# Performance work log

Measured on AMD Instinct MI355X. Metric: run time of the kernel, lower is better.

The kernel has to match this reference:

```python
import jax, jax.numpy as jnp
import numpy as np

B, S, D, H = 4, 2048, 512, 8
HD = D // H  # head dim = 64


def setup_inputs() -> dict:
    key = jax.random.key(0)
    ks = jax.random.split(key, 7)
    s = 0.02
    return {
        "X": jax.random.normal(ks[0], (B, S, D), dtype=jnp.float32),
        "Y": jax.random.normal(ks[1], (B, S, D), dtype=jnp.float32),
        "Z": jax.random.normal(ks[2], (B, S, D), dtype=jnp.float32),
        # weights stored as [in, out] (torch Linear weight transposed)
        "Wq": jax.random.normal(ks[3], (D, D), dtype=jnp.float32) * s,
        "Wk": jax.random.normal(ks[4], (D, D), dtype=jnp.float32) * s,
        "Wv": jax.random.normal(ks[5], (D, D), dtype=jnp.float32) * s,  # dead in original forward
        "Wo": jax.random.normal(ks[6], (D, D), dtype=jnp.float32) * s,
    }


def _split_heads(t):
    # [B, S, D] -> [B, H, S, HD]
    return t.reshape(B, S, H, HD).transpose(0, 2, 1, 3)


def reference(X, Y, Z, Wq, Wk, Wv, Wo):
    q = _split_heads(X @ Wq)
    k = _split_heads(Y @ Wk)
    # NOTE: original module (faithfully) uses W_o for the value projection; W_v is unused.
    v = _split_heads(Z @ Wo)
    scores = jnp.einsum("bhqd,bhkd->bhqk", q, k) / jnp.sqrt(jnp.float32(HD))
    # sigmoid(s) > 0.5  <=>  s > 0 (sigmoid strictly monotone); keep score else 0
    scores = jnp.where(scores > 0, scores, jnp.float32(0))
    attn = jax.nn.softmax(scores, axis=-1)
    out = jnp.einsum("bhqk,bhkd->bhqd", attn, v)  # dropout inactive at eval
    out = out.transpose(0, 2, 1, 3).reshape(B, S, D)  # merge heads
    return out @ Wo
```

## Files before the change

### kernel.cpp

```cpp
#include <hip/hip_runtime.h>
#include <math.h>

#define S_LEN 2048
#define DIM   512
#define M_TOT 8192
#define NCH   (S_LEN / 64)

typedef __attribute__((ext_vector_type(8))) short bf16x8;
typedef __attribute__((ext_vector_type(4))) short bf16x4;
typedef __attribute__((ext_vector_type(4))) float f32x4;

#define MFMA(a, b, c) __builtin_amdgcn_mfma_f32_16x16x32_bf16((a), (b), (c), 0, 0, 0)

#define QSCALE 0.18033688011112042f

__device__ __forceinline__ short f2b(float x) {
    union { float f; unsigned u; } v; v.f = x;
    unsigned r = v.u + 0x7FFFu + ((v.u >> 16) & 1u);
    return (short)(r >> 16);
}

__device__ __forceinline__ unsigned cvtpk(float a, float b) {
    unsigned r;
    asm("v_cvt_pk_bf16_f32 %0, %1, %2" : "=v"(r) : "v"(a), "v"(b));
    return r;
}

__device__ __forceinline__ bf16x8 cvt8(float4 lo, float4 hi) {
    union { unsigned u[4]; bf16x8 v; } o;
    o.u[0] = cvtpk(lo.x, lo.y);
    o.u[1] = cvtpk(lo.z, lo.w);
    o.u[2] = cvtpk(hi.x, hi.y);
    o.u[3] = cvtpk(hi.z, hi.w);
    return o.v;
}

__device__ __forceinline__ float fast_exp2(float x) {
#if __has_builtin(__builtin_amdgcn_exp2f)
    return __builtin_amdgcn_exp2f(x);
#else
    return __expf(x * 0.693147180559945f);
#endif
}

__global__ __launch_bounds__(256) void prep_wt(const float* Wq, const float* Wk, const float* Wo,
                                               short* Wtq, short* Wtk, short* Wto) {
    const int zi = blockIdx.z;
    const float* W = zi == 0 ? Wq : zi == 1 ? Wk : Wo;
    short*      Wt = zi == 0 ? Wtq : zi == 1 ? Wtk : Wto;
    const float sc = zi == 0 ? QSCALE : 1.0f;
    __shared__ short Ts[64 * 72];
    const int t = threadIdx.x;
    const int k0 = blockIdx.x * 64, n0 = blockIdx.y * 64;
    #pragma unroll
    for (int it = 0; it < 4; ++it) {
        const int r = (t >> 4) + 16 * it;
        const int cq = t & 15;
        float4 v = *(const float4*)&W[(size_t)(k0 + r) * DIM + n0 + cq * 4];
        Ts[(4 * cq + 0) * 72 + r] = f2b(v.x * sc);
        Ts[(4 * cq + 1) * 72 + r] = f2b(v.y * sc);
        Ts[(4 * cq + 2) * 72 + r] = f2b(v.z * sc);
        Ts[(4 * cq + 3) * 72 + r] = f2b(v.w * sc);
    }
    __syncthreads();
    #pragma unroll
    for (int it = 0; it < 2; ++it) {
        const int n = (t >> 3) + 32 * it;
        const int sg = t & 7;
        *(bf16x8*)&Wt[(size_t)(n0 + n) * DIM + k0 + sg * 8] = *(const bf16x8*)&Ts[n * 72 + sg * 8];
    }
}

__global__ __launch_bounds__(256) void proj_gemm(const float* __restrict__ X,
                                                 const float* __restrict__ Y,
                                                 const float* __restrict__ Z,
                                                 const short* __restrict__ Wtq,
                                                 const short* __restrict__ Wtk,
                                                 const short* __restrict__ Wto,
                                                 short* __restrict__ Qb,
                                                 short* __restrict__ Kb,
                                                 short* __restrict__ Vt) {
    const int zi = blockIdx.z;
    const float* A  = zi == 0 ? X : zi == 1 ? Y : Z;
    const short* Bw = zi == 0 ? Wtq : zi == 1 ? Wtk : Wto;

    __shared__ short As[128 * 40];
    __shared__ short Bs[128 * 40];
    const int tid = threadIdx.x;
    const int w = tid >> 6, ln = tid & 63, l15 = ln & 15, quad = ln >> 4;
    const int m0 = blockIdx.x * 128, n0 = blockIdx.y * 128;
    const int wm = (w & 1) * 64, wn = (w >> 1) * 64;

    const int r0 = tid >> 2, r1 = r0 + 64;
    const int sg = tid & 3;
    const float* ap0 = A  + (size_t)(m0 + r0) * DIM + sg * 8;
    const float* ap1 = A  + (size_t)(m0 + r1) * DIM + sg * 8;
    const short* bp0 = Bw + (size_t)(n0 + r0) * DIM + sg * 8;
    const short* bp1 = Bw + (size_t)(n0 + r1) * DIM + sg * 8;

    float4 a0l = *(const float4*)ap0, a0h = *(const float4*)(ap0 + 4);
    float4 a1l = *(const float4*)ap1, a1h = *(const float4*)(ap1 + 4);
    bf16x8 b0 = *(const bf16x8*)bp0, b1 = *(const bf16x8*)bp1;

    f32x4 acc[4][4] = {};

    for (int k0 = 0; k0 < DIM; k0 += 32) {
        __syncthreads();
        *(bf16x8*)&As[r0 * 40 + sg * 8] = cvt8(a0l, a0h);
        *(bf16x8*)&As[r1 * 40 + sg * 8] = cvt8(a1l, a1h);
        *(bf16x8*)&Bs[r0 * 40 + sg * 8] = b0;
        *(bf16x8*)&Bs[r1 * 40 + sg * 8] = b1;
        __syncthreads();
        const int kn = (k0 + 32 < DIM) ? k0 + 32 : 0;
        a0l = *(const float4*)(ap0 + kn); a0h = *(const float4*)(ap0 + kn + 4);
        a1l = *(const float4*)(ap1 + kn); a1h = *(const float4*)(ap1 + kn + 4);
        b0 = *(const bf16x8*)(bp0 + kn); b1 = *(const bf16x8*)(bp1 + kn);

        bf16x8 af[4], bf[4];
        #pragma unroll
        for (int mf = 0; mf < 4; ++mf) af[mf] = *(const bf16x8*)&As[(wm + 16 * mf + l15) * 40 + quad * 8];
        #pragma unroll
        for (int nf = 0; nf < 4; ++nf) bf[nf] = *(const bf16x8*)&Bs[(wn + 16 * nf + l15) * 40 + quad * 8];
        #pragma unroll
        for (int mf = 0; mf < 4; ++mf)
            #pragma unroll
            for (int nf = 0; nf < 4; ++nf)
                acc[mf][nf] = MFMA(af[mf], bf[nf], acc[mf][nf]);
    }

    if (zi < 2) {
        short* C = zi == 0 ? Qb : Kb;
        #pragma unroll
        for (int mf = 0; mf < 4; ++mf)
            #pragma unroll
            for (int nf = 0; nf < 4; ++nf)
                #pragma unroll
                for (int r = 0; r < 4; ++r)
                    C[(size_t)(m0 + wm + 16 * mf + 4 * quad + r) * DIM + n0 + wn + 16 * nf + l15] =
                        f2b(acc[mf][nf][r]);
    } else {
        #pragma unroll
        for (int mf = 0; mf < 4; ++mf)
            #pragma unroll
            for (int nf = 0; nf < 4; ++nf) {
                const int col = n0 + wn + 16 * nf + l15;
                const int h = col >> 6, hd = col & 63;
                const int row0_ = m0 + wm + 16 * mf + 4 * quad;
                const int bb = row0_ >> 11, s0 = row0_ & 2047;
                bf16x4 o = { f2b(acc[mf][nf][0]), f2b(acc[mf][nf][1]),
                             f2b(acc[mf][nf][2]), f2b(acc[mf][nf][3]) };
                *(bf16x4*)&Vt[((size_t)((bb * 8 + h) * 64 + hd)) * S_LEN + s0] = o;
            }
    }
}

__global__ __launch_bounds__(256) void out_gemm(const short* __restrict__ Ob,
                                                const short* __restrict__ Wto,
                                                float* __restrict__ Cout) {
    __shared__ short As[128 * 40];
    __shared__ short Bs[128 * 40];
    const int tid = threadIdx.x;
    const int w = tid >> 6, ln = tid & 63, l15 = ln & 15, quad = ln >> 4;
    const int m0 = blockIdx.x * 128, n0 = blockIdx.y * 128;
    const int wm = (w & 1) * 64, wn = (w >> 1) * 64;

    const int r0 = tid >> 2, r1 = r0 + 64;
    const int sg = tid & 3;
    const short* ap0 = Ob  + (size_t)(m0 + r0) * DIM + sg * 8;
    const short* ap1 = Ob  + (size_t)(m0 + r1) * DIM + sg * 8;
    const short* bp0 = Wto + (size_t)(n0 + r0) * DIM + sg * 8;
    const short* bp1 = Wto + (size_t)(n0 + r1) * DIM + sg * 8;

    bf16x8 a0 = *(const bf16x8*)ap0, a1 = *(const bf16x8*)ap1;
    bf16x8 b0 = *(const bf16x8*)bp0, b1 = *(const bf16x8*)bp1;

    f32x4 acc[4][4] = {};

    for (int k0 = 0; k0 < DIM; k0 += 32) {
        __syncthreads();
        *(bf16x8*)&As[r0 * 40 + sg * 8] = a0;
        *(bf16x8*)&As[r1 * 40 + sg * 8] = a1;
        *(bf16x8*)&Bs[r0 * 40 + sg * 8] = b0;
        *(bf16x8*)&Bs[r1 * 40 + sg * 8] = b1;
        __syncthreads();
        const int kn = (k0 + 32 < DIM) ? k0 + 32 : 0;
        a0 = *(const bf16x8*)(ap0 + kn); a1 = *(const bf16x8*)(ap1 + kn);
        b0 = *(const bf16x8*)(bp0 + kn); b1 = *(const bf16x8*)(bp1 + kn);

        bf16x8 af[4], bf[4];
        #pragma unroll
        for (int mf = 0; mf < 4; ++mf) af[mf] = *(const bf16x8*)&As[(wm + 16 * mf + l15) * 40 + quad * 8];
        #pragma unroll
        for (int nf = 0; nf < 4; ++nf) bf[nf] = *(const bf16x8*)&Bs[(wn + 16 * nf + l15) * 40 + quad * 8];
        #pragma unroll
        for (int mf = 0; mf < 4; ++mf)
            #pragma unroll
            for (int nf = 0; nf < 4; ++nf)
                acc[mf][nf] = MFMA(af[mf], bf[nf], acc[mf][nf]);
    }
    #pragma unroll
    for (int mf = 0; mf < 4; ++mf)
        #pragma unroll
        for (int nf = 0; nf < 4; ++nf)
            #pragma unroll
            for (int r = 0; r < 4; ++r)
                Cout[(size_t)(m0 + wm + 16 * mf + 4 * quad + r) * DIM + n0 + wn + 16 * nf + l15] =
                    acc[mf][nf][r];
}

__global__ __launch_bounds__(256) void attn_mfma(const short* __restrict__ Qb,
                                                 const short* __restrict__ Kb,
                                                 const short* __restrict__ Vtg,
                                                 short* __restrict__ Ob) {
    __shared__ short Ks[2][64 * 72];
    __shared__ short Vs[2][64 * 72];
    __shared__ short Es[4][32 * 72];

    const int tid = threadIdx.x;
    const int w = tid >> 6, ln = tid & 63, l15 = ln & 15, quad = ln >> 4;

    const int lin = blockIdx.y * 16 + blockIdx.x;
    const int swz = ((lin & 7) << 6) + (lin >> 3);
    const int qt0 = (swz & 15) * 128;
    const int bh  = swz >> 4;
    const int b = bh >> 3, h = bh & 7;
    const size_t tokbase = (size_t)b * S_LEN;

    bf16x8 qf[2][2];
    #pragma unroll
    for (int nf = 0; nf < 2; ++nf)
        #pragma unroll
        for (int ks = 0; ks < 2; ++ks)
            qf[nf][ks] = *(const bf16x8*)&Qb[(tokbase + qt0 + 32 * w + 16 * nf + l15) * DIM +
                                             h * 64 + 32 * ks + 8 * quad];

    const int srow = tid >> 3, ssg = tid & 7;
    const short* kbase = Kb  + (tokbase + srow) * DIM + h * 64 + ssg * 8;
    const short* vbase = Vtg + ((size_t)bh * 64 + srow) * S_LEN + ssg * 8;

    bf16x8 k0r, k1r, v0r, v1r;

    f32x4 oacc[2][4] = {};
    f32x4 d4[2] = {};

    {
        k0r = *(const bf16x8*)kbase;
        k1r = *(const bf16x8*)(kbase + (size_t)32 * DIM);
        v0r = *(const bf16x8*)vbase;
        v1r = *(const bf16x8*)(vbase + (size_t)32 * S_LEN);
        *(bf16x8*)&Ks[0][srow * 72 + ssg * 8] = k0r;
        *(bf16x8*)&Ks[0][(srow + 32) * 72 + ssg * 8] = k1r;
        *(bf16x8*)&Vs[0][srow * 72 + ssg * 8] = v0r;
        *(bf16x8*)&Vs[0][(srow + 32) * 72 + ssg * 8] = v1r;
        k0r = *(const bf16x8*)(kbase + (size_t)64 * DIM);
        k1r = *(const bf16x8*)(kbase + (size_t)96 * DIM);
        v0r = *(const bf16x8*)(vbase + 64);
        v1r = *(const bf16x8*)(vbase + (size_t)32 * S_LEN + 64);
    }
    __syncthreads();

    for (int kc = 0; kc < NCH; ++kc) {
        const int cur = kc & 1;
        if (kc + 1 < NCH) {
            *(bf16x8*)&Ks[cur ^ 1][srow * 72 + ssg * 8] = k0r;
            *(bf16x8*)&Ks[cur ^ 1][(srow + 32) * 72 + ssg * 8] = k1r;
            *(bf16x8*)&Vs[cur ^ 1][srow * 72 + ssg * 8] = v0r;
            *(bf16x8*)&Vs[cur ^ 1][(srow + 32) * 72 + ssg * 8] = v1r;
        }
        if (kc + 2 < NCH) {
            const size_t ko = (size_t)(kc + 2) * 64 * DIM;
            const size_t vo = (size_t)(kc + 2) * 64;
            k0r = *(const bf16x8*)(kbase + ko);
            k1r = *(const bf16x8*)(kbase + ko + (size_t)32 * DIM);
            v0r = *(const bf16x8*)(vbase + vo);
            v1r = *(const bf16x8*)(vbase + vo + (size_t)32 * S_LEN);
        }

        f32x4 sacc[4][2];
        __builtin_amdgcn_s_setprio(1);
        #pragma unroll
        for (int mf = 0; mf < 4; ++mf) {
            bf16x8 ka = *(const bf16x8*)&Ks[cur][(16 * mf + l15) * 72 + 8 * quad];
            bf16x8 kb = *(const bf16x8*)&Ks[cur][(16 * mf + l15) * 72 + 32 + 8 * quad];
            #pragma unroll
            for (int nf = 0; nf < 2; ++nf) {
                f32x4 s = {0.f, 0.f, 0.f, 0.f};
                s = MFMA(ka, qf[nf][0], s);
                s = MFMA(kb, qf[nf][1], s);
                sacc[mf][nf] = s;
            }
        }
        __builtin_amdgcn_s_setprio(0);

        short* Esw = &Es[w][0];
        #pragma unroll
        for (int mf = 0; mf < 4; ++mf)
            #pragma unroll
            for (int nf = 0; nf < 2; ++nf) {
                const float e0 = fast_exp2(fmaxf(sacc[mf][nf][0], 0.f));
                const float e1 = fast_exp2(fmaxf(sacc[mf][nf][1], 0.f));
                const float e2 = fast_exp2(fmaxf(sacc[mf][nf][2], 0.f));
                const float e3 = fast_exp2(fmaxf(sacc[mf][nf][3], 0.f));
                d4[nf][0] += e0; d4[nf][1] += e1;
                d4[nf][2] += e2; d4[nf][3] += e3;
                uint2 p;
                p.x = cvtpk(e0, e1);
                p.y = cvtpk(e2, e3);
                *(uint2*)&Esw[(16 * nf + l15) * 72 + 16 * mf + 4 * quad] = p;
            }

        bf16x8 e00 = *(const bf16x8*)&Esw[l15 * 72 + 8 * quad];
        bf16x8 e01 = *(const bf16x8*)&Esw[l15 * 72 + 32 + 8 * quad];
        bf16x8 e10 = *(const bf16x8*)&Esw[(16 + l15) * 72 + 8 * quad];
        bf16x8 e11 = *(const bf16x8*)&Esw[(16 + l15) * 72 + 32 + 8 * quad];
        __builtin_amdgcn_s_setprio(1);
        #pragma unroll
        for (int nf2 = 0; nf2 < 4; ++nf2) {
            bf16x8 vf0 = *(const bf16x8*)&Vs[cur][(16 * nf2 + l15) * 72 + 8 * quad];
            bf16x8 vf1 = *(const bf16x8*)&Vs[cur][(16 * nf2 + l15) * 72 + 32 + 8 * quad];
            oacc[0][nf2] = MFMA(e00, vf0, oacc[0][nf2]);
            oacc[0][nf2] = MFMA(e01, vf1, oacc[0][nf2]);
            oacc[1][nf2] = MFMA(e10, vf0, oacc[1][nf2]);
            oacc[1][nf2] = MFMA(e11, vf1, oacc[1][nf2]);
        }
        __builtin_amdgcn_s_setprio(0);
        __syncthreads();
    }

    float dsum[2];
    #pragma unroll
    for (int nf = 0; nf < 2; ++nf) {
        dsum[nf] = (d4[nf][0] + d4[nf][1]) + (d4[nf][2] + d4[nf][3]);
        dsum[nf] += __shfl_xor(dsum[nf], 16);
        dsum[nf] += __shfl_xor(dsum[nf], 32);
    }
    const float dinv0 = 1.0f / dsum[0];
    const float dinv1 = 1.0f / dsum[1];

    #pragma unroll
    for (int mf2 = 0; mf2 < 2; ++mf2) {
        const float dv = mf2 ? dinv1 : dinv0;
        #pragma unroll
        for (int r = 0; r < 4; ++r) {
            const float di = __shfl(dv, 4 * quad + r);
            const size_t rowaddr = (tokbase + qt0 + 32 * w + 16 * mf2 + 4 * quad + r) * DIM + h * 64;
            #pragma unroll
            for (int nf2 = 0; nf2 < 4; ++nf2)
                Ob[rowaddr + 16 * nf2 + l15] = f2b(oacc[mf2][nf2][r] * di);
        }
    }
}

extern "C" void kernel_launch(void* const* d_in, const int* in_sizes, int n_in,
                              void* d_out, int out_size, void* d_ws, size_t ws_size,
                              hipStream_t stream) {
    const float* X  = (const float*)d_in[0];
    const float* Y  = (const float*)d_in[1];
    const float* Z  = (const float*)d_in[2];
    const float* Wq = (const float*)d_in[3];
    const float* Wk = (const float*)d_in[4];
    const float* Wo = (const float*)d_in[6];

    char* p = (char*)d_ws;
    const size_t MD = (size_t)M_TOT * DIM;
    short* Qb  = (short*)p; p += MD * 2;
    short* Kb  = (short*)p; p += MD * 2;
    short* Vt  = (short*)p; p += MD * 2;
    short* Ob  = (short*)p; p += MD * 2;
    short* Wtq = (short*)p; p += (size_t)DIM * DIM * 2;
    short* Wtk = (short*)p; p += (size_t)DIM * DIM * 2;
    short* Wto = (short*)p; p += (size_t)DIM * DIM * 2;

    prep_wt<<<dim3(8, 8, 3), 256, 0, stream>>>(Wq, Wk, Wo, Wtq, Wtk, Wto);
    proj_gemm<<<dim3(64, 4, 3), 256, 0, stream>>>(X, Y, Z, Wtq, Wtk, Wto, Qb, Kb, Vt);
    attn_mfma<<<dim3(16, 32), 256, 0, stream>>>(Qb, Kb, Vt, Ob);
    out_gemm<<<dim3(64, 4), 256, 0, stream>>>(Ob, Wto, (float*)d_out);
}
```

Before: 208.7 us.

## Halve attention and output GEMM tiles to double grid size, drop LDS double-buffering

The attention kernel now gives each block 64 queries instead of 128 (16 per wave), launching 1024 blocks with a 1D swizzled index, and replaces the double-buffered K/V shared tiles with a single buffer plus a register prefetch one chunk ahead. The output GEMM tile shrinks from 128x128 to 64x64 with 1024 swizzled blocks. This is meant to raise occupancy and fill the CUs better with less LDS and fewer registers per block. In exchange, each K/V tile is loaded from global twice as often per query, MFMA work per LDS read drops, and removing the double buffer exposes load latency at each barrier.

```diff
diff --git a/kernel.cpp b/kernel.cpp
--- a/kernel.cpp
+++ b/kernel.cpp
@@ -157,51 +157,48 @@
 __global__ __launch_bounds__(256) void out_gemm(const short* __restrict__ Ob,
                                                 const short* __restrict__ Wto,
                                                 float* __restrict__ Cout) {
-    __shared__ short As[128 * 40];
-    __shared__ short Bs[128 * 40];
+    __shared__ short As[64 * 40];
+    __shared__ short Bs[64 * 40];
     const int tid = threadIdx.x;
     const int w = tid >> 6, ln = tid & 63, l15 = ln & 15, quad = ln >> 4;
-    const int m0 = blockIdx.x * 128, n0 = blockIdx.y * 128;
-    const int wm = (w & 1) * 64, wn = (w >> 1) * 64;
-
-    const int r0 = tid >> 2, r1 = r0 + 64;
+
+    const int f = blockIdx.x;
+    const int swz = ((f & 7) << 7) | (f >> 3);
+    const int m0 = (swz >> 3) * 64, n0 = (swz & 7) * 64;
+    const int wm = (w & 1) * 32, wn = (w >> 1) * 32;
+
+    const int row = tid >> 2;
     const int sg = tid & 3;
-    const short* ap0 = Ob  + (size_t)(m0 + r0) * DIM + sg * 8;
-    const short* ap1 = Ob  + (size_t)(m0 + r1) * DIM + sg * 8;
-    const short* bp0 = Wto + (size_t)(n0 + r0) * DIM + sg * 8;
-    const short* bp1 = Wto + (size_t)(n0 + r1) * DIM + sg * 8;
-
-    bf16x8 a0 = *(const bf16x8*)ap0, a1 = *(const bf16x8*)ap1;
-    bf16x8 b0 = *(const bf16x8*)bp0, b1 = *(const bf16x8*)bp1;
-
-    f32x4 acc[4][4] = {};
+    const short* ap = Ob  + (size_t)(m0 + row) * DIM + sg * 8;
+    const short* bp = Wto + (size_t)(n0 + row) * DIM + sg * 8;
+
+    bf16x8 a0 = *(const bf16x8*)ap, b0 = *(const bf16x8*)bp;
+
+    f32x4 acc[2][2] = {};
 
     for (int k0 = 0; k0 < DIM; k0 += 32) {
         __syncthreads();
-        *(bf16x8*)&As[r0 * 40 + sg * 8] = a0;
-        *(bf16x8*)&As[r1 * 40 + sg * 8] = a1;
-        *(bf16x8*)&Bs[r0 * 40 + sg * 8] = b0;
-        *(bf16x8*)&Bs[r1 * 40 + sg * 8] = b1;
+        *(bf16x8*)&As[row * 40 + sg * 8] = a0;
+        *(bf16x8*)&Bs[row * 40 + sg * 8] = b0;
         __syncthreads();
         const int kn = (k0 + 32 < DIM) ? k0 + 32 : 0;
-        a0 = *(const bf16x8*)(ap0 + kn); a1 = *(const bf16x8*)(ap1 + kn);
-        b0 = *(const bf16x8*)(bp0 + kn); b1 = *(const bf16x8*)(bp1 + kn);
-
-        bf16x8 af[4], bf[4];
-        #pragma unroll
-        for (int mf = 0; mf < 4; ++mf) af[mf] = *(const bf16x8*)&As[(wm + 16 * mf + l15) * 40 + quad * 8];
-        #pragma unroll
-        for (int nf = 0; nf < 4; ++nf) bf[nf] = *(const bf16x8*)&Bs[(wn + 16 * nf + l15) * 40 + quad * 8];
-        #pragma unroll
-        for (int mf = 0; mf < 4; ++mf)
-            #pragma unroll
-            for (int nf = 0; nf < 4; ++nf)
+        a0 = *(const bf16x8*)(ap + kn); b0 = *(const bf16x8*)(bp + kn);
+
+        bf16x8 af[2], bf[2];
+        #pragma unroll
+        for (int mf = 0; mf < 2; ++mf) af[mf] = *(const bf16x8*)&As[(wm + 16 * mf + l15) * 40 + quad * 8];
+        #pragma unroll
+        for (int nf = 0; nf < 2; ++nf) bf[nf] = *(const bf16x8*)&Bs[(wn + 16 * nf + l15) * 40 + quad * 8];
+        #pragma unroll
+        for (int mf = 0; mf < 2; ++mf)
+            #pragma unroll
+            for (int nf = 0; nf < 2; ++nf)
                 acc[mf][nf] = MFMA(af[mf], bf[nf], acc[mf][nf]);
     }
     #pragma unroll
-    for (int mf = 0; mf < 4; ++mf)
-        #pragma unroll
-        for (int nf = 0; nf < 4; ++nf)
+    for (int mf = 0; mf < 2; ++mf)
+        #pragma unroll
+        for (int nf = 0; nf < 2; ++nf)
             #pragma unroll
             for (int r = 0; r < 4; ++r)
                 Cout[(size_t)(m0 + wm + 16 * mf + 4 * quad + r) * DIM + n0 + wn + 16 * nf + l15] =
@@ -212,142 +209,106 @@
                                                  const short* __restrict__ Kb,
                                                  const short* __restrict__ Vtg,
                                                  short* __restrict__ Ob) {
-    __shared__ short Ks[2][64 * 72];
-    __shared__ short Vs[2][64 * 72];
-    __shared__ short Es[4][32 * 72];
+    __shared__ short Ks[64 * 72];
+    __shared__ short Vs[64 * 72];
+    __shared__ short Es[4][16 * 72];
 
     const int tid = threadIdx.x;
     const int w = tid >> 6, ln = tid & 63, l15 = ln & 15, quad = ln >> 4;
 
-    const int lin = blockIdx.y * 16 + blockIdx.x;
-    const int swz = ((lin & 7) << 6) + (lin >> 3);
-    const int qt0 = (swz & 15) * 128;
-    const int bh  = swz >> 4;
+    const int f = blockIdx.x;
+    const int swz = ((f & 7) << 7) | (f >> 3);
+    const int qt0 = (swz & 31) * 64;
+    const int bh  = swz >> 5;
     const int b = bh >> 3, h = bh & 7;
     const size_t tokbase = (size_t)b * S_LEN;
 
-    bf16x8 qf[2][2];
-    #pragma unroll
-    for (int nf = 0; nf < 2; ++nf)
-        #pragma unroll
-        for (int ks = 0; ks < 2; ++ks)
-            qf[nf][ks] = *(const bf16x8*)&Qb[(tokbase + qt0 + 32 * w + 16 * nf + l15) * DIM +
-                                             h * 64 + 32 * ks + 8 * quad];
+    bf16x8 qf[2];
+    #pragma unroll
+    for (int ks = 0; ks < 2; ++ks)
+        qf[ks] = *(const bf16x8*)&Qb[(tokbase + qt0 + 16 * w + l15) * DIM +
+                                     h * 64 + 32 * ks + 8 * quad];
 
     const int srow = tid >> 3, ssg = tid & 7;
     const short* kbase = Kb  + (tokbase + srow) * DIM + h * 64 + ssg * 8;
     const short* vbase = Vtg + ((size_t)bh * 64 + srow) * S_LEN + ssg * 8;
 
-    bf16x8 k0r, k1r, v0r, v1r;
-
-    f32x4 oacc[2][4] = {};
-    f32x4 d4[2] = {};
-
-    {
-        k0r = *(const bf16x8*)kbase;
-        k1r = *(const bf16x8*)(kbase + (size_t)32 * DIM);
-        v0r = *(const bf16x8*)vbase;
-        v1r = *(const bf16x8*)(vbase + (size_t)32 * S_LEN);
-        *(bf16x8*)&Ks[0][srow * 72 + ssg * 8] = k0r;
-        *(bf16x8*)&Ks[0][(srow + 32) * 72 + ssg * 8] = k1r;
-        *(bf16x8*)&Vs[0][srow * 72 + ssg * 8] = v0r;
-        *(bf16x8*)&Vs[0][(srow + 32) * 72 + ssg * 8] = v1r;
-        k0r = *(const bf16x8*)(kbase + (size_t)64 * DIM);
-        k1r = *(const bf16x8*)(kbase + (size_t)96 * DIM);
-        v0r = *(const bf16x8*)(vbase + 64);
-        v1r = *(const bf16x8*)(vbase + (size_t)32 * S_LEN + 64);
-    }
-    __syncthreads();
+    bf16x8 k0r = *(const bf16x8*)kbase;
+    bf16x8 k1r = *(const bf16x8*)(kbase + (size_t)32 * DIM);
+    bf16x8 v0r = *(const bf16x8*)vbase;
+    bf16x8 v1r = *(const bf16x8*)(vbase + (size_t)32 * S_LEN);
+
+    f32x4 oacc[4] = {};
+    f32x4 d4 = {0.f, 0.f, 0.f, 0.f};
 
     for (int kc = 0; kc < NCH; ++kc) {
-        const int cur = kc & 1;
+        *(bf16x8*)&Ks[srow * 72 + ssg * 8] = k0r;
+        *(bf16x8*)&Ks[(srow + 32) * 72 + ssg * 8] = k1r;
+        *(bf16x8*)&Vs[srow * 72 + ssg * 8] = v0r;
+        *(bf16x8*)&Vs[(srow + 32) * 72 + ssg * 8] = v1r;
+        __syncthreads();
         if (kc + 1 < NCH) {
-            *(bf16x8*)&Ks[cur ^ 1][srow * 72 + ssg * 8] = k0r;
-            *(bf16x8*)&Ks[cur ^ 1][(srow + 32) * 72 + ssg * 8] = k1r;
-            *(bf16x8*)&Vs[cur ^ 1][srow * 72 + ssg * 8] = v0r;
-            *(bf16x8*)&Vs[cur ^ 1][(srow + 32) * 72 + ssg * 8] = v1r;
-        }
-        if (kc + 2 < NCH) {
-            const size_t ko = (size_t)(kc + 2) * 64 * DIM;
-            const size_t vo = (size_t)(kc + 2) * 64;
+            const size_t ko = (size_t)(kc + 1) * 64 * DIM;
+            const size_t vo = (size_t)(kc + 1) * 64;
             k0r = *(const bf16x8*)(kbase + ko);
             k1r = *(const bf16x8*)(kbase + ko + (size_t)32 * DIM);
             v0r = *(const bf16x8*)(vbase + vo);
             v1r = *(const bf16x8*)(vbase + vo + (size_t)32 * S_LEN);
         }
 
-        f32x4 sacc[4][2];
+        f32x4 sacc[4];
         __builtin_amdgcn_s_setprio(1);
         #pragma unroll
         for (int mf = 0; mf < 4; ++mf) {
-            bf16x8 ka = *(const bf16x8*)&Ks[cur][(16 * mf + l15) * 72 + 8 * quad];
-            bf16x8 kb = *(const bf16x8*)&Ks[cur][(16 * mf + l15) * 72 + 32 + 8 * quad];
-            #pragma unroll
-            for (int nf = 0; nf < 2; ++nf) {
-                f32x4 s = {0.f, 0.f, 0.f, 0.f};
-                s = MFMA(ka, qf[nf][0], s);
-                s = MFMA(kb, qf[nf][1], s);
-                sacc[mf][nf] = s;
-            }
+            bf16x8 ka = *(const bf16x8*)&Ks[(16 * mf + l15) * 72 + 8 * quad];
+            bf16x8 kb = *(const bf16x8*)&Ks[(16 * mf + l15) * 72 + 32 + 8 * quad];
+            f32x4 s = {0.f, 0.f, 0.f, 0.f};
+            s = MFMA(ka, qf[0], s);
+            s = MFMA(kb, qf[1], s);
+            sacc[mf] = s;
         }
         __builtin_amdgcn_s_setprio(0);
 
         short* Esw = &Es[w][0];
         #pragma unroll
-        for (int mf = 0; mf < 4; ++mf)
-            #pragma unroll
-            for (int nf = 0; nf < 2; ++nf) {
-                const float e0 = fast_exp2(fmaxf(sacc[mf][nf][0], 0.f));
-                const float e1 = fast_exp2(fmaxf(sacc[mf][nf][1], 0.f));
-                const float e2 = fast_exp2(fmaxf(sacc[mf][nf][2], 0.f));
-                const float e3 = fast_exp2(fmaxf(sacc[mf][nf][3], 0.f));
-                d4[nf][0] += e0; d4[nf][1] += e1;
-                d4[nf][2] += e2; d4[nf][3] += e3;
-                uint2 p;
-                p.x = cvtpk(e0, e1);
-                p.y = cvtpk(e2, e3);
-                *(uint2*)&Esw[(16 * nf + l15) * 72 + 16 * mf + 4 * quad] = p;
-            }
-
-        bf16x8 e00 = *(const bf16x8*)&Esw[l15 * 72 + 8 * quad];
-        bf16x8 e01 = *(const bf16x8*)&Esw[l15 * 72 + 32 + 8 * quad];
-        bf16x8 e10 = *(const bf16x8*)&Esw[(16 + l15) * 72 + 8 * quad];
-        bf16x8 e11 = *(const bf16x8*)&Esw[(16 + l15) * 72 + 32 + 8 * quad];
+        for (int mf = 0; mf < 4; ++mf) {
+            const float e0 = fast_exp2(fmaxf(sacc[mf][0], 0.f));
+            const float e1 = fast_exp2(fmaxf(sacc[mf][1], 0.f));
+            const float e2 = fast_exp2(fmaxf(sacc[mf][2], 0.f));
+            const float e3 = fast_exp2(fmaxf(sacc[mf][3], 0.f));
+            d4[0] += e0; d4[1] += e1; d4[2] += e2; d4[3] += e3;
+            uint2 p;
+            p.x = cvtpk(e0, e1);
+            p.y = cvtpk(e2, e3);
+            *(uint2*)&Esw[l15 * 72 + 16 * mf + 4 * quad] = p;
+        }
+
+        bf16x8 e0 = *(const bf16x8*)&Esw[l15 * 72 + 8 * quad];
+        bf16x8 e1 = *(const bf16x8*)&Esw[l15 * 72 + 32 + 8 * quad];
         __builtin_amdgcn_s_setprio(1);
         #pragma unroll
         for (int nf2 = 0; nf2 < 4; ++nf2) {
-            bf16x8 vf0 = *(const bf16x8*)&Vs[cur][(16 * nf2 + l15) * 72 + 8 * quad];
-            bf16x8 vf1 = *(const bf16x8*)&Vs[cur][(16 * nf2 + l15) * 72 + 32 + 8 * quad];
-            oacc[0][nf2] = MFMA(e00, vf0, oacc[0][nf2]);
-            oacc[0][nf2] = MFMA(e01, vf1, oacc[0][nf2]);
-            oacc[1][nf2] = MFMA(e10, vf0, oacc[1][nf2]);
-            oacc[1][nf2] = MFMA(e11, vf1, oacc[1][nf2]);
+            bf16x8 vf0 = *(const bf16x8*)&Vs[(16 * nf2 + l15) * 72 + 8 * quad];
+            bf16x8 vf1 = *(const bf16x8*)&Vs[(16 * nf2 + l15) * 72 + 32 + 8 * quad];
+            oacc[nf2] = MFMA(e0, vf0, oacc[nf2]);
+            oacc[nf2] = MFMA(e1, vf1, oacc[nf2]);
         }
         __builtin_amdgcn_s_setprio(0);
         __syncthreads();
     }
 
-    float dsum[2];
-    #pragma unroll
-    for (int nf = 0; nf < 2; ++nf) {
-        dsum[nf] = (d4[nf][0] + d4[nf][1]) + (d4[nf][2] + d4[nf][3]);
-        dsum[nf] += __shfl_xor(dsum[nf], 16);
-        dsum[nf] += __shfl_xor(dsum[nf], 32);
-    }
-    const float dinv0 = 1.0f / dsum[0];
-    const float dinv1 = 1.0f / dsum[1];
-
-    #pragma unroll
-    for (int mf2 = 0; mf2 < 2; ++mf2) {
-        const float dv = mf2 ? dinv1 : dinv0;
-        #pragma unroll
-        for (int r = 0; r < 4; ++r) {
-            const float di = __shfl(dv, 4 * quad + r);
-            const size_t rowaddr = (tokbase + qt0 + 32 * w + 16 * mf2 + 4 * quad + r) * DIM + h * 64;
-            #pragma unroll
-            for (int nf2 = 0; nf2 < 4; ++nf2)
-                Ob[rowaddr + 16 * nf2 + l15] = f2b(oacc[mf2][nf2][r] * di);
-        }
+    float dsum = (d4[0] + d4[1]) + (d4[2] + d4[3]);
+    dsum += __shfl_xor(dsum, 16);
+    dsum += __shfl_xor(dsum, 32);
+    const float dinv = 1.0f / dsum;
+
+    #pragma unroll
+    for (int r = 0; r < 4; ++r) {
+        const float di = __shfl(dinv, 4 * quad + r);
+        const size_t rowaddr = (tokbase + qt0 + 16 * w + 4 * quad + r) * DIM + h * 64;
+        #pragma unroll
+        for (int nf2 = 0; nf2 < 4; ++nf2)
+            Ob[rowaddr + 16 * nf2 + l15] = f2b(oacc[nf2][r] * di);
     }
 }
 
@@ -373,6 +334,6 @@
 
     prep_wt<<<dim3(8, 8, 3), 256, 0, stream>>>(Wq, Wk, Wo, Wtq, Wtk, Wto);
     proj_gemm<<<dim3(64, 4, 3), 256, 0, stream>>>(X, Y, Z, Wtq, Wtk, Wto, Qb, Kb, Vt);
-    attn_mfma<<<dim3(16, 32), 256, 0, stream>>>(Qb, Kb, Vt, Ob);
-    out_gemm<<<dim3(64, 4), 256, 0, stream>>>(Ob, Wto, (float*)d_out);
-}
+    attn_mfma<<<dim3(1024), 256, 0, stream>>>(Qb, Kb, Vt, Ob);
+    out_gemm<<<dim3(1024), 256, 0, stream>>>(Ob, Wto, (float*)d_out);
+}
```

New measurement: 203.8 us. -2.3%, faster.
